# Kernel tuning notes

Measured on AMD Instinct MI355X. Metric: run time of the kernel, lower is better.

## Reference

```python
import jax, jax.numpy as jnp
import numpy as np

N = 50000   # nodes
E = 1600000 # edges (avg degree 32)
D = 128     # in_feats
H = 128     # n_hidden
C = 47      # n_classes


def setup_inputs() -> dict:
    key = jax.random.key(0)
    ks = jax.random.split(key, 10)
    w = lambda k, i, o: jax.random.normal(k, (i, o), jnp.float32) * 0.05
    return {
        "feat": jax.random.normal(ks[0], (N, D), jnp.float32),
        "src": jax.random.randint(ks[1], (E,), 0, N),
        "dst": jax.random.randint(ks[2], (E,), 0, N),
        "Wself0": w(ks[3], D, H), "Wneigh0": w(ks[4], D, H), "b0": jnp.zeros((H,), jnp.float32),
        "Wself1": w(ks[5], H, H), "Wneigh1": w(ks[6], H, H), "b1": jnp.zeros((H,), jnp.float32),
        "Wfc": w(ks[7], H, C), "bfc": jnp.zeros((C,), jnp.float32),
    }


def _sage_mean(feat, src, dst, Wself, Wneigh, b):
    # gather source features along edges, segment-mean into destination nodes
    msgs = feat[src]                                              # [E, d]
    agg = jax.ops.segment_sum(msgs, dst, num_segments=N)          # [N, d]
    deg = jax.ops.segment_sum(jnp.ones((E,), feat.dtype), dst, num_segments=N)
    h_neigh = agg / jnp.maximum(deg, 1.0)[:, None]                # mean, deg-0 safe
    return feat @ Wself + h_neigh @ Wneigh + b


def reference(feat, src, dst, Wself0, Wneigh0, b0, Wself1, Wneigh1, b1, Wfc, bfc):
    h = jax.nn.relu(_sage_mean(feat, src, dst, Wself0, Wneigh0, b0))
    h = jax.nn.relu(_sage_mean(h, src, dst, Wself1, Wneigh1, b1))
    return h @ Wfc + bfc
```

## Files before the change

### kernel.cpp

```cpp
#include <hip/hip_runtime.h>

#define NN 50000
#define NE 1600000
#define NBA 128
#define CPB (NE / NBA)
#define NBUCK 196
#define MAXBE 12288

typedef unsigned int uint;
typedef __attribute__((ext_vector_type(8))) short short8;
typedef __attribute__((ext_vector_type(4))) float f32x4;
typedef __attribute__((ext_vector_type(4), aligned(4))) float f32x4u;


__device__ __forceinline__ uint bf16rne(float f) {
  uint u = __float_as_uint(f);
  return (u + 0x7fffu + ((u >> 16) & 1u)) >> 16;
}
__device__ __forceinline__ uint packbf2(float lo, float hi) {
  return bf16rne(lo) | (bf16rne(hi) << 16);
}
__device__ __forceinline__ float bflo(uint u) { return __uint_as_float(u << 16); }
__device__ __forceinline__ float bfhi(uint u) { return __uint_as_float(u & 0xffff0000u); }

__device__ __forceinline__ short8 as_short8(uint4 v) {
  union { uint4 u; short8 s; } cv; cv.u = v; return cv.s;
}

__device__ __forceinline__ void add8(const uint4 v, float* a) {
  a[0] += bflo(v.x); a[1] += bfhi(v.x);
  a[2] += bflo(v.y); a[3] += bfhi(v.y);
  a[4] += bflo(v.z); a[5] += bfhi(v.z);
  a[6] += bflo(v.w); a[7] += bfhi(v.w);
}

__global__ __launch_bounds__(256) void tobf16_kernel(const float* __restrict__ in,
                                                     uint* __restrict__ outb, int n8) {
  int t = blockIdx.x * 256 + threadIdx.x;
  if (t < n8) {
    float4 a = ((const float4*)in)[2 * t];
    float4 b = ((const float4*)in)[2 * t + 1];
    uint4 o;
    o.x = packbf2(a.x, a.y);
    o.y = packbf2(a.z, a.w);
    o.z = packbf2(b.x, b.y);
    o.w = packbf2(b.z, b.w);
    ((uint4*)outb)[t] = o;
  }
}


__global__ __launch_bounds__(256) void packW_kernel(const float* __restrict__ W00,
                                                    const float* __restrict__ W01,
                                                    const float* __restrict__ W10,
                                                    const float* __restrict__ W11,
                                                    const float* __restrict__ Wfc,
                                                    uint4* __restrict__ Wpack) {
  int t = blockIdx.x * 256 + threadIdx.x;
  if (t < 16384) {
    int lane = t & 63;
    int ks   = (t >> 6) & 3;
    int ft   = (t >> 8) & 7;
    int part = (t >> 11) & 1;
    int mat  = (t >> 12) & 1;
    int layer= (t >> 13) & 1;
    const float* Wsrc = layer ? (mat ? W11 : W10) : (mat ? W01 : W00);
    int feat  = ft * 16 + (lane & 15);
    int kbase = ks * 32 + (lane >> 4) * 8;
    uint o[4];
#pragma unroll
    for (int h = 0; h < 4; ++h) {
      float w0 = Wsrc[(kbase + 2 * h) * 128 + feat];
      float w1 = Wsrc[(kbase + 2 * h + 1) * 128 + feat];
      uint h0 = bf16rne(w0), h1 = bf16rne(w1);
      uint v0, v1;
      if (part == 0) { v0 = h0; v1 = h1; }
      else {
        v0 = bf16rne(w0 - __uint_as_float(h0 << 16));
        v1 = bf16rne(w1 - __uint_as_float(h1 << 16));
      }
      o[h] = v0 | (v1 << 16);
    }
    uint4 r; r.x = o[0]; r.y = o[1]; r.z = o[2]; r.w = o[3];
    Wpack[t] = r;
  } else if (t < 16384 + 1536) {
    int tt = t - 16384;
    int lane = tt & 63;
    int ks   = (tt >> 6) & 3;
    int ct   = (tt >> 8) % 3;
    int part = tt / 768;
    int col  = ct * 16 + (lane & 15);
    int kbase = ks * 32 + (lane >> 4) * 8;
    uint o[4];
#pragma unroll
    for (int h = 0; h < 4; ++h) {
      float w0 = (col < 47) ? Wfc[(kbase + 2 * h) * 47 + col] : 0.f;
      float w1 = (col < 47) ? Wfc[(kbase + 2 * h + 1) * 47 + col] : 0.f;
      uint h0 = bf16rne(w0), h1 = bf16rne(w1);
      uint v0, v1;
      if (part == 0) { v0 = h0; v1 = h1; }
      else {
        v0 = bf16rne(w0 - __uint_as_float(h0 << 16));
        v1 = bf16rne(w1 - __uint_as_float(h1 << 16));
      }
      o[h] = v0 | (v1 << 16);
    }
    uint4 r; r.x = o[0]; r.y = o[1]; r.z = o[2]; r.w = o[3];
    Wpack[t] = r;
  }
}


__global__ __launch_bounds__(1024) void histA_kernel(const int* __restrict__ dst,
                                                     int* __restrict__ histA) {
  __shared__ int h[NBUCK];
  int tid = threadIdx.x, b = blockIdx.x;
  if (tid < NBUCK) h[tid] = 0;
  __syncthreads();
  const int4* d4 = (const int4*)(dst + b * CPB);
  for (int i = tid; i < CPB / 4; i += 1024) {
    int4 d = d4[i];
    atomicAdd(&h[d.x >> 8], 1);
    atomicAdd(&h[d.y >> 8], 1);
    atomicAdd(&h[d.z >> 8], 1);
    atomicAdd(&h[d.w >> 8], 1);
  }
  __syncthreads();
  if (tid < NBUCK) histA[b * NBUCK + tid] = h[tid];
}

__global__ __launch_bounds__(256) void scanA_kernel(int* __restrict__ histA,
                                                    int* __restrict__ bucket_base) {
  __shared__ int wsum[4];
  int t = threadIdx.x;
  int s = 0;
  if (t < NBUCK) {
#pragma unroll 8
    for (int b = 0; b < NBA; ++b) {
      int v = histA[b * NBUCK + t];
      histA[b * NBUCK + t] = s;
      s += v;
    }
  }
  int lane = t & 63, wid = t >> 6;
  int x = s;
#pragma unroll
  for (int d = 1; d < 64; d <<= 1) {
    int y = __shfl_up(x, d, 64);
    if (lane >= d) x += y;
  }
  if (lane == 63) wsum[wid] = x;
  __syncthreads();
  int woff = 0;
  if (wid > 0) woff += wsum[0];
  if (wid > 1) woff += wsum[1];
  if (wid > 2) woff += wsum[2];
  int excl = woff + x - s;
  if (t < NBUCK) bucket_base[t] = excl;
  if (t == NBUCK - 1) bucket_base[NBUCK] = excl + s;
}

__global__ __launch_bounds__(1024) void scatterA_kernel(const int* __restrict__ src,
                                                        const int* __restrict__ dst,
                                                        const int* __restrict__ histA,
                                                        const int* __restrict__ bucket_base,
                                                        uint* __restrict__ gbuf) {
  __shared__ int cur[NBUCK];
  int tid = threadIdx.x, b = blockIdx.x;
  if (tid < NBUCK) cur[tid] = histA[b * NBUCK + tid] + bucket_base[tid];
  __syncthreads();
  const int4* d4 = (const int4*)(dst + b * CPB);
  const int4* s4 = (const int4*)(src + b * CPB);
  for (int i = tid; i < CPB / 4; i += 1024) {
    int4 d = d4[i];
    int4 s = s4[i];
    int p0 = atomicAdd(&cur[d.x >> 8], 1);
    int p1 = atomicAdd(&cur[d.y >> 8], 1);
    int p2 = atomicAdd(&cur[d.z >> 8], 1);
    int p3 = atomicAdd(&cur[d.w >> 8], 1);
    gbuf[p0] = (uint)s.x | ((uint)(d.x & 255) << 16);
    gbuf[p1] = (uint)s.y | ((uint)(d.y & 255) << 16);
    gbuf[p2] = (uint)s.z | ((uint)(d.z & 255) << 16);
    gbuf[p3] = (uint)s.w | ((uint)(d.w & 255) << 16);
  }
}

__global__ __launch_bounds__(1024) void passB_kernel(const uint* __restrict__ gbuf,
                                                     const int* __restrict__ bucket_base,
                                                     int* __restrict__ offs,
                                                     int* __restrict__ csr) {
  __shared__ int cnt_l[256];
  __shared__ int cur_l[256];
  __shared__ int wsum[4];
  int tid = threadIdx.x, b = blockIdx.x;
  int bbase = bucket_base[b];
  int nE = bucket_base[b + 1] - bbase;
  int lo = b << 8;
  if (tid < 256) cnt_l[tid] = 0;
  __syncthreads();

  const uint* gptr = gbuf + bbase;
  uint pv[MAXBE / 1024];
#pragma unroll
  for (int j = 0; j < MAXBE / 1024; ++j) {
    int i = tid + j * 1024;
    if (i < nE) {
      uint p = gptr[i];
      pv[j] = p;
      atomicAdd(&cnt_l[(p >> 16) & 255], 1);
    }
  }
  __syncthreads();

  int excl = 0, v = 0;
  if (tid < 256) {
    v = cnt_l[tid];
    int lane = tid & 63, wid = tid >> 6;
    int x = v;
#pragma unroll
    for (int d = 1; d < 64; d <<= 1) {
      int y = __shfl_up(x, d, 64);
      if (lane >= d) x += y;
    }
    if (lane == 63) wsum[wid] = x;
    __syncthreads();
    int woff = 0;
    if (wid > 0) woff += wsum[0];
    if (wid > 1) woff += wsum[1];
    if (wid > 2) woff += wsum[2];
    excl = woff + x - v;
    cur_l[tid] = excl;
    int node = lo + tid;
    if (node <= NN) offs[node] = bbase + excl;
  } else {
    __syncthreads();
  }
  __syncthreads();

#pragma unroll
  for (int j = 0; j < MAXBE / 1024; ++j) {
    int i = tid + j * 1024;
    if (i < nE) {
      uint p = pv[j];
      int r = atomicAdd(&cur_l[(p >> 16) & 255], 1);
      csr[bbase + r] = (int)(p & 0xFFFFu);
    }
  }
}


__global__ __launch_bounds__(256) void agg_kernel(const uint* __restrict__ Xb,
                                                  const int* __restrict__ csr,
                                                  const int* __restrict__ offs,
                                                  uint* __restrict__ outb, int N) {
  const uint4* __restrict__ X4 = (const uint4*)Xb;
  int tid = threadIdx.x;
  int slot = tid >> 4;
  int lane = tid & 15;
  int n = blockIdx.x * 16 + slot;
  if (n >= N) return;
  int s = offs[n], e = offs[n + 1];

  float aA[8] = {0.f, 0.f, 0.f, 0.f, 0.f, 0.f, 0.f, 0.f};
  float aB[8] = {0.f, 0.f, 0.f, 0.f, 0.f, 0.f, 0.f, 0.f};

  int j = s;
  for (; j + 8 <= e; j += 8) {
    int i0 = csr[j + 0], i1 = csr[j + 1], i2 = csr[j + 2], i3 = csr[j + 3];
    int i4 = csr[j + 4], i5 = csr[j + 5], i6 = csr[j + 6], i7 = csr[j + 7];
    uint4 v0 = X4[i0 * 16 + lane];
    uint4 v1 = X4[i1 * 16 + lane];
    uint4 v2 = X4[i2 * 16 + lane];
    uint4 v3 = X4[i3 * 16 + lane];
    uint4 v4 = X4[i4 * 16 + lane];
    uint4 v5 = X4[i5 * 16 + lane];
    uint4 v6 = X4[i6 * 16 + lane];
    uint4 v7 = X4[i7 * 16 + lane];
    add8(v0, aA); add8(v1, aA); add8(v2, aA); add8(v3, aA);
    add8(v4, aB); add8(v5, aB); add8(v6, aB); add8(v7, aB);
  }
  for (; j < e; ++j) {
    uint4 v = X4[csr[j] * 16 + lane];
    add8(v, aA);
  }

  float inv = 1.0f / fmaxf((float)(e - s), 1.0f);
  uint4 o;
  o.x = packbf2((aA[0] + aB[0]) * inv, (aA[1] + aB[1]) * inv);
  o.y = packbf2((aA[2] + aB[2]) * inv, (aA[3] + aB[3]) * inv);
  o.z = packbf2((aA[4] + aB[4]) * inv, (aA[5] + aB[5]) * inv);
  o.w = packbf2((aA[6] + aB[6]) * inv, (aA[7] + aB[7]) * inv);
  ((uint4*)outb)[n * 16 + lane] = o;
}


#define MFMA16(a, b, c) __builtin_amdgcn_mfma_f32_16x16x32_bf16((a), (b), (c), 0, 0, 0)

__global__ __launch_bounds__(512) void gemm_mfma(
    const uint* __restrict__ As_g, const uint* __restrict__ An_g,
    const uint4* __restrict__ Wp,
    const float* __restrict__ bias, uint* __restrict__ Out, int N) {
  __shared__ uint4 sT[2][16][17];
  int tid = threadIdx.x;
  int lane = tid & 63;
  int ft = tid >> 6;
  int ng = blockIdx.x;
  int l15 = lane & 15, lhi = lane >> 4;

  short8 aH[2][4], aL[2][4];
#pragma unroll
  for (int m = 0; m < 2; ++m)
#pragma unroll
    for (int ks = 0; ks < 4; ++ks) {
      aH[m][ks] = as_short8(Wp[(m * 2 + 0) * 2048 + ft * 256 + ks * 64 + lane]);
      aL[m][ks] = as_short8(Wp[(m * 2 + 1) * 2048 + ft * 256 + ks * 64 + lane]);
    }
  int feat0 = ft * 16 + lhi * 4;
  float bv0 = bias[feat0], bv1 = bias[feat0 + 1];
  float bv2 = bias[feat0 + 2], bv3 = bias[feat0 + 3];

  const uint4* __restrict__ Xs = (const uint4*)As_g;
  const uint4* __restrict__ Xn = (const uint4*)An_g;

  int smat = tid >> 8;
  int sidx = tid & 255;
  int srow = sidx >> 4;
  int scol = sidx & 15;

  for (int t = 0; t < 8; ++t) {
    int grow = ng * 128 + t * 16 + srow;
    if (grow >= N) grow = N - 1;
    const uint4* srcp = smat ? Xn : Xs;
    sT[smat][srow][scol] = srcp[grow * 16 + scol];
    __syncthreads();

    f32x4 acc = {0.f, 0.f, 0.f, 0.f};
    short8 b;
#pragma unroll
    for (int ks = 0; ks < 4; ++ks) {
      b = as_short8(sT[0][l15][ks * 4 + lhi]);
      acc = MFMA16(aH[0][ks], b, acc);
      acc = MFMA16(aL[0][ks], b, acc);
    }
#pragma unroll
    for (int ks = 0; ks < 4; ++ks) {
      b = as_short8(sT[1][l15][ks * 4 + lhi]);
      acc = MFMA16(aH[1][ks], b, acc);
      acc = MFMA16(aL[1][ks], b, acc);
    }

    int row = ng * 128 + t * 16 + l15;
    float o0 = fmaxf(acc[0] + bv0, 0.f);
    float o1 = fmaxf(acc[1] + bv1, 0.f);
    float o2 = fmaxf(acc[2] + bv2, 0.f);
    float o3 = fmaxf(acc[3] + bv3, 0.f);
    if (row < N) {
      uint2 st;
      st.x = packbf2(o0, o1);
      st.y = packbf2(o2, o3);
      ((uint2*)Out)[row * 32 + ft * 4 + lhi] = st;
    }
    __syncthreads();
  }
}


__global__ __launch_bounds__(256) void fc_mfma(const uint* __restrict__ Hb,
                                               const uint4* __restrict__ Wfcp,
                                               const float* __restrict__ bg,
                                               float* __restrict__ Out, int N) {
  int tid = threadIdx.x;
  int lane = tid & 63;
  int t = blockIdx.x * 4 + (tid >> 6);
  int l15 = lane & 15, lhi = lane >> 4;

  short8 aH[3][4], aL[3][4];
#pragma unroll
  for (int ct = 0; ct < 3; ++ct)
#pragma unroll
    for (int ks = 0; ks < 4; ++ks) {
      aH[ct][ks] = as_short8(Wfcp[((0 * 3 + ct) * 4 + ks) * 64 + lane]);
      aL[ct][ks] = as_short8(Wfcp[((1 * 3 + ct) * 4 + ks) * 64 + lane]);
    }

  int row = t * 16 + l15;
  int rr = row < N ? row : N - 1;
  const uint4* ph = ((const uint4*)Hb) + rr * 16 + lhi;
  uint4 b0 = ph[0], b1 = ph[4], b2 = ph[8], b3 = ph[12];
  short8 v0 = as_short8(b0), v1 = as_short8(b1), v2 = as_short8(b2), v3 = as_short8(b3);

  f32x4 acc[3];
#pragma unroll
  for (int ct = 0; ct < 3; ++ct) {
    f32x4 a = {0.f, 0.f, 0.f, 0.f};
    a = MFMA16(aH[ct][0], v0, a); a = MFMA16(aL[ct][0], v0, a);
    a = MFMA16(aH[ct][1], v1, a); a = MFMA16(aL[ct][1], v1, a);
    a = MFMA16(aH[ct][2], v2, a); a = MFMA16(aL[ct][2], v2, a);
    a = MFMA16(aH[ct][3], v3, a); a = MFMA16(aL[ct][3], v3, a);
    acc[ct] = a;
  }

  if (row < N) {
    float* orow = Out + (size_t)row * 47;
#pragma unroll
    for (int ct = 0; ct < 3; ++ct) {
      int col0 = ct * 16 + lhi * 4;
      if (col0 + 3 < 47) {
        f32x4u st;
        st[0] = acc[ct][0] + bg[col0];
        st[1] = acc[ct][1] + bg[col0 + 1];
        st[2] = acc[ct][2] + bg[col0 + 2];
        st[3] = acc[ct][3] + bg[col0 + 3];
        *(f32x4u*)(orow + col0) = st;
      } else {
#pragma unroll
        for (int r = 0; r < 4; ++r) {
          int col = col0 + r;
          if (col < 47) orow[col] = acc[ct][r] + bg[col];
        }
      }
    }
  }
}


extern "C" void kernel_launch(void* const* d_in, const int* in_sizes, int n_in,
                              void* d_out, int out_size, void* d_ws, size_t ws_size,
                              hipStream_t stream) {
  const float* feat    = (const float*)d_in[0];
  const int*   src     = (const int*)d_in[1];
  const int*   dst     = (const int*)d_in[2];
  const float* Wself0  = (const float*)d_in[3];
  const float* Wneigh0 = (const float*)d_in[4];
  const float* b0      = (const float*)d_in[5];
  const float* Wself1  = (const float*)d_in[6];
  const float* Wneigh1 = (const float*)d_in[7];
  const float* b1      = (const float*)d_in[8];
  const float* Wfc     = (const float*)d_in[9];
  const float* bfc     = (const float*)d_in[10];
  float* out = (float*)d_out;

  char* w = (char*)d_ws;
  int*   offs    = (int*)(w);
  int*   bbase   = (int*)(w + 262144);
  int*   histA   = (int*)(w + 266240);
  int*   csr     = (int*)(w + 524288);
  uint4* Wpack   = (uint4*)(w + 7340032);
  uint*  featb   = (uint*)(w + 7864320);
  uint*  h2b     = (uint*)(w + 7864320);
  uint*  gbuf    = (uint*)(w + 20971520);
  uint*  hnb     = (uint*)(w + 27787264);
  uint*  h0b     = (uint*)(w + 41943040);

  const int N = NN;

  histA_kernel<<<NBA, 1024, 0, stream>>>(dst, histA);
  scanA_kernel<<<1, 256, 0, stream>>>(histA, bbase);
  scatterA_kernel<<<NBA, 1024, 0, stream>>>(src, dst, histA, bbase, gbuf);
  passB_kernel<<<NBUCK, 1024, 0, stream>>>(gbuf, bbase, offs, csr);

  tobf16_kernel<<<(N * 16 + 255) / 256, 256, 0, stream>>>(feat, featb, N * 16);
  packW_kernel<<<70, 256, 0, stream>>>(Wself0, Wneigh0, Wself1, Wneigh1, Wfc, Wpack);

  const int gblocks = (N + 127) / 128;
  const int fcblocks = ((N + 15) / 16 + 3) / 4;

  agg_kernel<<<(N + 15) / 16, 256, 0, stream>>>(featb, csr, offs, hnb, N);
  gemm_mfma<<<gblocks, 512, 0, stream>>>(featb, hnb, Wpack, b0, h0b, N);
  agg_kernel<<<(N + 15) / 16, 256, 0, stream>>>(h0b, csr, offs, hnb, N);
  gemm_mfma<<<gblocks, 512, 0, stream>>>(h0b, hnb, Wpack + 8192, b1, h2b, N);
  fc_mfma<<<fcblocks, 256, 0, stream>>>(h2b, Wpack + 16384, bfc, out, N);
}
```

Before: 187.0 us.

## Fuse final FC layer into second GEMM via shared memory, retune histogram blocks

The second SAGE layer's GEMM now keeps its 128-row bf16 output tile in shared memory and runs the 47-class FC projection in the same kernel. This removes the separate fc_mfma launch and the global write and re-read of the hidden activations. The edge-histogram block count also changes from 128 to 200. In exchange, the added shared-memory buffer and FC weight registers in gemm_mfma may reduce occupancy.

Result: faster. 183.0 us (-2.1%).

```diff
diff --git a/kernel.cpp b/kernel.cpp
--- a/kernel.cpp
+++ b/kernel.cpp
@@ -2,7 +2,7 @@
 
 #define NN 50000
 #define NE 1600000
-#define NBA 128
+#define NBA 200
 #define CPB (NE / NBA)
 #define NBUCK 196
 #define MAXBE 12288
@@ -299,8 +299,11 @@
 __global__ __launch_bounds__(512) void gemm_mfma(
     const uint* __restrict__ As_g, const uint* __restrict__ An_g,
     const uint4* __restrict__ Wp,
-    const float* __restrict__ bias, uint* __restrict__ Out, int N) {
+    const float* __restrict__ bias, uint* __restrict__ Out,
+    const uint4* __restrict__ Wfcp, const float* __restrict__ bfc,
+    float* __restrict__ OutFC, int do_fc, int N) {
   __shared__ uint4 sT[2][16][17];
+  __shared__ uint4 h2s[128][17];
   int tid = threadIdx.x;
   int lane = tid & 63;
   int ft = tid >> 6;
@@ -349,74 +352,68 @@
       acc = MFMA16(aL[1][ks], b, acc);
     }
 
-    int row = ng * 128 + t * 16 + l15;
+    int rloc = t * 16 + l15;
+    int row = ng * 128 + rloc;
     float o0 = fmaxf(acc[0] + bv0, 0.f);
     float o1 = fmaxf(acc[1] + bv1, 0.f);
     float o2 = fmaxf(acc[2] + bv2, 0.f);
     float o3 = fmaxf(acc[3] + bv3, 0.f);
+    uint2 st;
+    st.x = packbf2(o0, o1);
+    st.y = packbf2(o2, o3);
+    if (do_fc) {
+      ((uint2*)&h2s[rloc][0])[ft * 4 + lhi] = st;
+    } else if (row < N) {
+      ((uint2*)Out)[row * 32 + ft * 4 + lhi] = st;
+    }
+    __syncthreads();
+  }
+
+  if (do_fc) {
+    short8 fH[3][4], fL[3][4];
+#pragma unroll
+    for (int ct = 0; ct < 3; ++ct)
+#pragma unroll
+      for (int ks = 0; ks < 4; ++ks) {
+        fH[ct][ks] = as_short8(Wfcp[((0 * 3 + ct) * 4 + ks) * 64 + lane]);
+        fL[ct][ks] = as_short8(Wfcp[((1 * 3 + ct) * 4 + ks) * 64 + lane]);
+      }
+    int rloc = ft * 16 + l15;
+    int row = ng * 128 + rloc;
+    short8 v0 = as_short8(h2s[rloc][0 * 4 + lhi]);
+    short8 v1 = as_short8(h2s[rloc][1 * 4 + lhi]);
+    short8 v2 = as_short8(h2s[rloc][2 * 4 + lhi]);
+    short8 v3 = as_short8(h2s[rloc][3 * 4 + lhi]);
+
+    f32x4 facc[3];
+#pragma unroll
+    for (int ct = 0; ct < 3; ++ct) {
+      f32x4 a = {0.f, 0.f, 0.f, 0.f};
+      a = MFMA16(fH[ct][0], v0, a); a = MFMA16(fL[ct][0], v0, a);
+      a = MFMA16(fH[ct][1], v1, a); a = MFMA16(fL[ct][1], v1, a);
+      a = MFMA16(fH[ct][2], v2, a); a = MFMA16(fL[ct][2], v2, a);
+      a = MFMA16(fH[ct][3], v3, a); a = MFMA16(fL[ct][3], v3, a);
+      facc[ct] = a;
+    }
+
     if (row < N) {
-      uint2 st;
-      st.x = packbf2(o0, o1);
-      st.y = packbf2(o2, o3);
-      ((uint2*)Out)[row * 32 + ft * 4 + lhi] = st;
-    }
-    __syncthreads();
-  }
-}
-
-
-__global__ __launch_bounds__(256) void fc_mfma(const uint* __restrict__ Hb,
-                                               const uint4* __restrict__ Wfcp,
-                                               const float* __restrict__ bg,
-                                               float* __restrict__ Out, int N) {
-  int tid = threadIdx.x;
-  int lane = tid & 63;
-  int t = blockIdx.x * 4 + (tid >> 6);
-  int l15 = lane & 15, lhi = lane >> 4;
-
-  short8 aH[3][4], aL[3][4];
-#pragma unroll
-  for (int ct = 0; ct < 3; ++ct)
-#pragma unroll
-    for (int ks = 0; ks < 4; ++ks) {
-      aH[ct][ks] = as_short8(Wfcp[((0 * 3 + ct) * 4 + ks) * 64 + lane]);
-      aL[ct][ks] = as_short8(Wfcp[((1 * 3 + ct) * 4 + ks) * 64 + lane]);
-    }
-
-  int row = t * 16 + l15;
-  int rr = row < N ? row : N - 1;
-  const uint4* ph = ((const uint4*)Hb) + rr * 16 + lhi;
-  uint4 b0 = ph[0], b1 = ph[4], b2 = ph[8], b3 = ph[12];
-  short8 v0 = as_short8(b0), v1 = as_short8(b1), v2 = as_short8(b2), v3 = as_short8(b3);
-
-  f32x4 acc[3];
-#pragma unroll
-  for (int ct = 0; ct < 3; ++ct) {
-    f32x4 a = {0.f, 0.f, 0.f, 0.f};
-    a = MFMA16(aH[ct][0], v0, a); a = MFMA16(aL[ct][0], v0, a);
-    a = MFMA16(aH[ct][1], v1, a); a = MFMA16(aL[ct][1], v1, a);
-    a = MFMA16(aH[ct][2], v2, a); a = MFMA16(aL[ct][2], v2, a);
-    a = MFMA16(aH[ct][3], v3, a); a = MFMA16(aL[ct][3], v3, a);
-    acc[ct] = a;
-  }
-
-  if (row < N) {
-    float* orow = Out + (size_t)row * 47;
-#pragma unroll
-    for (int ct = 0; ct < 3; ++ct) {
-      int col0 = ct * 16 + lhi * 4;
-      if (col0 + 3 < 47) {
-        f32x4u st;
-        st[0] = acc[ct][0] + bg[col0];
-        st[1] = acc[ct][1] + bg[col0 + 1];
-        st[2] = acc[ct][2] + bg[col0 + 2];
-        st[3] = acc[ct][3] + bg[col0 + 3];
-        *(f32x4u*)(orow + col0) = st;
-      } else {
-#pragma unroll
-        for (int r = 0; r < 4; ++r) {
-          int col = col0 + r;
-          if (col < 47) orow[col] = acc[ct][r] + bg[col];
+      float* orow = OutFC + (size_t)row * 47;
+#pragma unroll
+      for (int ct = 0; ct < 3; ++ct) {
+        int col0 = ct * 16 + lhi * 4;
+        if (col0 + 3 < 47) {
+          f32x4u stv;
+          stv[0] = facc[ct][0] + bfc[col0];
+          stv[1] = facc[ct][1] + bfc[col0 + 1];
+          stv[2] = facc[ct][2] + bfc[col0 + 2];
+          stv[3] = facc[ct][3] + bfc[col0 + 3];
+          *(f32x4u*)(orow + col0) = stv;
+        } else {
+#pragma unroll
+          for (int r = 0; r < 4; ++r) {
+            int col = col0 + r;
+            if (col < 47) orow[col] = facc[ct][r] + bfc[col];
+          }
         }
       }
     }
@@ -447,7 +444,6 @@
   int*   csr     = (int*)(w + 524288);
   uint4* Wpack   = (uint4*)(w + 7340032);
   uint*  featb   = (uint*)(w + 7864320);
-  uint*  h2b     = (uint*)(w + 7864320);
   uint*  gbuf    = (uint*)(w + 20971520);
   uint*  hnb     = (uint*)(w + 27787264);
   uint*  h0b     = (uint*)(w + 41943040);
@@ -463,11 +459,11 @@
   packW_kernel<<<70, 256, 0, stream>>>(Wself0, Wneigh0, Wself1, Wneigh1, Wfc, Wpack);
 
   const int gblocks = (N + 127) / 128;
-  const int fcblocks = ((N + 15) / 16 + 3) / 4;
 
   agg_kernel<<<(N + 15) / 16, 256, 0, stream>>>(featb, csr, offs, hnb, N);
-  gemm_mfma<<<gblocks, 512, 0, stream>>>(featb, hnb, Wpack, b0, h0b, N);
+  gemm_mfma<<<gblocks, 512, 0, stream>>>(featb, hnb, Wpack, b0, h0b,
+                                         Wpack + 16384, bfc, out, 0, N);
   agg_kernel<<<(N + 15) / 16, 256, 0, stream>>>(h0b, csr, offs, hnb, N);
-  gemm_mfma<<<gblocks, 512, 0, stream>>>(h0b, hnb, Wpack + 8192, b1, h2b, N);
-  fc_mfma<<<fcblocks, 256, 0, stream>>>(h2b, Wpack + 16384, bfc, out, N);
-}
+  gemm_mfma<<<gblocks, 512, 0, stream>>>(h0b, hnb, Wpack + 8192, b1, h0b,
+                                         Wpack + 16384, bfc, out, 1, N);
+}
```
